# Performance work log

Measured on AMD Instinct MI355X. Metric: run time of the kernel, lower is better.

The kernel has to match this reference:

```python
import jax, jax.numpy as jnp
import numpy as np

B, S, D, H = 4, 2048, 1024, 16
HD = D // H

def setup_inputs() -> dict:
    key = jax.random.key(0)
    ks = jax.random.split(key, 10)
    s = 1.0 / np.sqrt(D)
    inp = {
        'x': jax.random.normal(ks[0], (B, S, D), dtype=jnp.float32),
        'attention_mask': jnp.ones((B, S), dtype=jnp.int32),
        'Wq': jax.random.uniform(ks[1], (D, D), jnp.float32, -s, s),
        'bq': jax.random.uniform(ks[2], (D,), jnp.float32, -s, s),
        'Wk': jax.random.uniform(ks[3], (D, D), jnp.float32, -s, s),
        'bk': jax.random.uniform(ks[4], (D,), jnp.float32, -s, s),
        'Wv': jax.random.uniform(ks[5], (D, D), jnp.float32, -s, s),
        'bv': jax.random.uniform(ks[6], (D,), jnp.float32, -s, s),
        'Wo': jax.random.uniform(ks[7], (D, D), jnp.float32, -s, s),
        'bo': jax.random.uniform(ks[8], (D,), jnp.float32, -s, s),
    }
    return inp

def reference(x, Wq, bq, Wk, bk, Wv, bv, Wo, bo, attention_mask):
    scale = HD ** -0.5
    # torch Linear: y = x @ W^T + b
    def proj(W, b):
        return (x @ W.T + b).reshape(B, S, H, HD).transpose(0, 2, 1, 3)  # [B,H,S,hd]
    q = proj(Wq, bq)
    k = proj(Wk, bk)
    v = proj(Wv, bv)
    scores = jnp.einsum('bhqd,bhkd->bhqk', q, k) * scale  # [B,H,S,S]
    causal = jnp.triu(jnp.ones((S, S), dtype=bool), k=1)
    scores = jnp.where(causal, -jnp.inf, scores)
    pad = (attention_mask == 0)[:, None, None, :]  # [B,1,1,S]
    scores = jnp.where(pad, jnp.float32(-1e9), scores)
    probs = jax.nn.softmax(scores, axis=-1)
    out = jnp.einsum('bhqk,bhkd->bhqd', probs, v)  # [B,H,S,hd]
    out = out.transpose(0, 2, 1, 3).reshape(B, S, D)
    return out @ Wo.T + bo
```

## Files before the change

kernel.cpp:

```cpp
#include <hip/hip_runtime.h>
#include <hip/hip_bf16.h>

typedef unsigned short u16;
typedef float f32x4 __attribute__((ext_vector_type(4)));
typedef __bf16 bf16x8 __attribute__((ext_vector_type(8)));

#define BB 4
#define SS 2048
#define DD 1024
#define HH 16
#define HDD 64
#define MM (BB*SS)

__device__ __forceinline__ u16 f2bf(float f){
    union { float f; unsigned int i; } v; v.f = f;
    unsigned int i = v.i;
    return (u16)((i + 0x7FFFu + ((i >> 16) & 1u)) >> 16);
}
__device__ __forceinline__ ushort2 pk2(float a, float b){
    union { __hip_bfloat162 h; ushort2 u; } v;
    float2 t; t.x = a; t.y = b;
    v.h = __float22bfloat162_rn(t);
    return v.u;
}
__device__ __forceinline__ ushort4 pk4(float a, float b, float c, float d){
    ushort2 lo = pk2(a, b), hi = pk2(c, d);
    ushort4 r; r.x = lo.x; r.y = lo.y; r.z = hi.x; r.w = hi.y;
    return r;
}
__device__ __forceinline__ void gl2lds16(const void* g, void* l){
    __builtin_amdgcn_global_load_lds(
        (const __attribute__((address_space(1))) void*)g,
        (__attribute__((address_space(3))) void*)l, 16, 0, 0);
}

__device__ __forceinline__ void cvt8(const float* __restrict__ src,
                                     u16* __restrict__ dst, size_t i)
{
    const float4 a = *(const float4*)&src[i];
    const float4 b = *(const float4*)&src[i + 4];
    ushort4 lo = pk4(a.x, a.y, a.z, a.w);
    ushort4 hi = pk4(b.x, b.y, b.z, b.w);
    uint4 o;
    o.x = (unsigned)lo.x | ((unsigned)lo.y << 16);
    o.y = (unsigned)lo.z | ((unsigned)lo.w << 16);
    o.z = (unsigned)hi.x | ((unsigned)hi.y << 16);
    o.w = (unsigned)hi.z | ((unsigned)hi.w << 16);
    *(uint4*)&dst[i] = o;
}

__global__ __launch_bounds__(256) void cvt_k(const float* __restrict__ src,
                                             u16* __restrict__ dst)
{
    const size_t i = ((size_t)blockIdx.x * 256 + threadIdx.x) * 8;
    cvt8(src, dst, i);
}

__global__ __launch_bounds__(256) void cvtw3_k(
    const float* __restrict__ W0, const float* __restrict__ W1,
    const float* __restrict__ W2, u16* __restrict__ dst)
{
    const float* src = blockIdx.y == 0 ? W0 : (blockIdx.y == 1 ? W1 : W2);
    u16* d = dst + (size_t)blockIdx.y * (size_t)DD * DD;
    const size_t i = ((size_t)blockIdx.x * 256 + threadIdx.x) * 8;
    cvt8(src, d, i);
}

__global__ __launch_bounds__(256) void cvtw1_k(const float* __restrict__ W,
                                               u16* __restrict__ dst)
{
    const size_t i = ((size_t)blockIdx.x * 256 + threadIdx.x) * 8;
    cvt8(W, dst, i);
}

__device__ __forceinline__ void gemm_core(const u16* __restrict__ Wb,
                                          const u16* __restrict__ Act,
                                          f32x4 (&acc)[4][4],
                                          u16 (&At)[2][256 * 32],
                                          u16 (&Bt)[2][128 * 32],
                                          int n0, int m0, int tid)
{
    const int lane = tid & 63, w = tid >> 6;
    const int quad = lane >> 4, l15 = lane & 15;
    const int wn2 = w & 3, wm2 = w >> 2;
    const int arow = lane >> 2;
    const int acol = (lane & 3) * 8;

    auto STG = [&](int bi, int kt) {
        const int kk = kt * 32;
        #pragma unroll
        for (int c0 = 0; c0 < 3; ++c0) {
            const int c = w * 3 + c0;
            if (c < 16) {
                gl2lds16(&Wb[(size_t)(n0 + c * 16 + arow) * DD + kk + acol],
                         &At[bi][c * 512]);
            } else {
                const int cb = c - 16;
                gl2lds16(&Act[(size_t)(m0 + cb * 16 + arow) * DD + kk + acol],
                         &Bt[bi][cb * 512]);
            }
        }
    };
    auto CMP = [&](int bi) {
        bf16x8 af[4], bfr[4];
        #pragma unroll
        for (int i = 0; i < 4; ++i)
            af[i] = *(const bf16x8*)&At[bi][(wn2 * 64 + i * 16 + l15) * 32 + quad * 8];
        #pragma unroll
        for (int j = 0; j < 4; ++j)
            bfr[j] = *(const bf16x8*)&Bt[bi][(wm2 * 64 + j * 16 + l15) * 32 + quad * 8];
        #pragma unroll
        for (int i = 0; i < 4; ++i)
            #pragma unroll
            for (int j = 0; j < 4; ++j)
                acc[i][j] = __builtin_amdgcn_mfma_f32_16x16x32_bf16(af[i], bfr[j], acc[i][j], 0, 0, 0);
    };

    STG(0, 0);
    __syncthreads();
    #pragma unroll 1
    for (int i = 0; i < 15; ++i) {
        STG(1, 2 * i + 1);
        CMP(0);
        __syncthreads();
        STG(0, 2 * i + 2);
        CMP(1);
        __syncthreads();
    }
    STG(1, 31);
    CMP(0);
    __syncthreads();
    CMP(1);
}

__global__ __launch_bounds__(512, 2) void gemm_qkv_k(
    const u16* __restrict__ x,
    const float* __restrict__ bq, const float* __restrict__ bk,
    const float* __restrict__ bv,
    const u16* __restrict__ Wqb, const u16* __restrict__ Wkb,
    const u16* __restrict__ Wvb,
    u16* __restrict__ Q, u16* __restrict__ K, u16* __restrict__ V)
{
    __shared__ alignas(16) u16 At[2][256 * 32];
    __shared__ alignas(16) u16 Bt[2][128 * 32];
    const int tid = threadIdx.x, lane = tid & 63, w = tid >> 6;
    const int quad = lane >> 4, l15 = lane & 15;
    const int wn2 = w & 3, wm2 = w >> 2;
    const int z = blockIdx.z;
    const u16* Wmb = z == 0 ? Wqb : (z == 1 ? Wkb : Wvb);
    const float* bias = z == 0 ? bq : (z == 1 ? bk : bv);
    u16* Out = z == 0 ? Q : (z == 1 ? K : V);
    const int m0 = blockIdx.x * 128, n0 = blockIdx.y * 256;

    f32x4 acc[4][4];
    #pragma unroll
    for (int i = 0; i < 4; ++i)
        #pragma unroll
        for (int j = 0; j < 4; ++j) acc[i][j] = (f32x4)(0.0f);

    gemm_core(Wmb, x, acc, At, Bt, n0, m0, tid);

    f32x4 bsv[4];
    #pragma unroll
    for (int i = 0; i < 4; ++i)
        bsv[i] = *(const f32x4*)&bias[n0 + wn2 * 64 + i * 16 + quad * 4];

    const int b = m0 / SS;
    const int h = (n0 + wn2 * 64) / HDD;
    const size_t base = ((size_t)(b * HH + h)) * SS * HDD;
    if (z == 2) {
        #pragma unroll
        for (int i = 0; i < 4; ++i) {
            #pragma unroll
            for (int r = 0; r < 4; ++r) {
                const int hd = i * 16 + quad * 4 + r;
                const float bb = bsv[i][r];
                #pragma unroll
                for (int j = 0; j < 4; ++j) {
                    const int s = (m0 % SS) + wm2 * 64 + j * 16 + l15;
                    Out[base + (size_t)hd * SS + s] = f2bf(acc[i][j][r] + bb);
                }
            }
        }
    } else {
        #pragma unroll
        for (int j = 0; j < 4; ++j) {
            const int s = (m0 % SS) + wm2 * 64 + j * 16 + l15;
            #pragma unroll
            for (int i = 0; i < 4; ++i) {
                *(ushort4*)&Out[base + (size_t)s * HDD + i * 16 + quad * 4] =
                    pk4(acc[i][j][0] + bsv[i][0], acc[i][j][1] + bsv[i][1],
                        acc[i][j][2] + bsv[i][2], acc[i][j][3] + bsv[i][3]);
            }
        }
    }
}

__global__ __launch_bounds__(512, 2) void gemm_out_k(
    const u16* __restrict__ A, const float* __restrict__ bo,
    const u16* __restrict__ Wob, float* __restrict__ Out)
{
    __shared__ alignas(16) u16 At[2][256 * 32];
    __shared__ alignas(16) u16 Bt[2][128 * 32];
    const int tid = threadIdx.x, lane = tid & 63, w = tid >> 6;
    const int quad = lane >> 4, l15 = lane & 15;
    const int wn2 = w & 3, wm2 = w >> 2;
    const int m0 = blockIdx.x * 128, n0 = blockIdx.y * 256;

    f32x4 acc[4][4];
    #pragma unroll
    for (int i = 0; i < 4; ++i)
        #pragma unroll
        for (int j = 0; j < 4; ++j) acc[i][j] = (f32x4)(0.0f);

    gemm_core(Wob, A, acc, At, Bt, n0, m0, tid);

    f32x4 bsv[4];
    #pragma unroll
    for (int i = 0; i < 4; ++i)
        bsv[i] = *(const f32x4*)&bo[n0 + wn2 * 64 + i * 16 + quad * 4];

    #pragma unroll
    for (int j = 0; j < 4; ++j) {
        const int m = m0 + wm2 * 64 + j * 16 + l15;
        #pragma unroll
        for (int i = 0; i < 4; ++i) {
            float4 f;
            f.x = acc[i][j][0] + bsv[i][0];
            f.y = acc[i][j][1] + bsv[i][1];
            f.z = acc[i][j][2] + bsv[i][2];
            f.w = acc[i][j][3] + bsv[i][3];
            *(float4*)&Out[(size_t)m * DD + n0 + wn2 * 64 + i * 16 + quad * 4] = f;
        }
    }
}

#define QT 128
#define KT 64

#define LOG2E 1.4426950408889634f

__device__ __forceinline__ int swz128(int row, int bcol){
    return row * 128 + (bcol ^ ((row & 7) << 4));
}

__global__ __launch_bounds__(256, 2) void attn_k(
    const u16* __restrict__ Q, const u16* __restrict__ K,
    const u16* __restrict__ V, const int* __restrict__ mask,
    u16* __restrict__ AO)
{
    __shared__ alignas(16) u16 QPs[QT * 64];
    __shared__ alignas(16) u16 Ks[KT * 64];
    __shared__ alignas(16) u16 Vs[KT * 64];
    __shared__ float padf[KT];

    const int tid = threadIdx.x, lane = tid & 63, w = tid >> 6;
    const int quad = lane >> 4, l15 = lane & 15;
    const int bh = blockIdx.x;
    const int y = blockIdx.y;
    const int qt = (y < 8) ? (15 - y) : (y - 8);
    const int b = bh >> 4, h = bh & 15;
    const int q0 = qt * QT;
    const size_t hoff = (size_t)bh * SS * HDD;
    const u16* Qh = Q + hoff;
    const u16* Kh = K + hoff;
    const u16* Vt = V + hoff;
    const int nkt = (q0 + QT) / KT;
    const float scale2 = 0.125f * LOG2E;
    const int wrow_end = q0 + w * 32 + 32;

    const int vrow = lane >> 3;
    const int dbcol = (((lane & 7) ^ vrow) << 4);

    for (int c = tid; c < QT * 8; c += 256) {
        const int row = c >> 3, cc = c & 7;
        *(uint4*)((char*)QPs + swz128(row, cc * 16)) =
            *(const uint4*)&Qh[(size_t)(q0 + row) * HDD + cc * 8];
    }
    __syncthreads();

    bf16x8 bQ[2][2];
    #pragma unroll
    for (int j = 0; j < 2; ++j)
        #pragma unroll
        for (int ks = 0; ks < 2; ++ks)
            bQ[j][ks] = *(const bf16x8*)((const char*)QPs +
                swz128(w * 32 + j * 16 + l15, ks * 64 + quad * 16));

    float m_run[2] = { -1e30f, -1e30f };
    float l_run[2] = { 0.f, 0.f };
    f32x4 o[4][2];
    #pragma unroll
    for (int i = 0; i < 4; ++i)
        #pragma unroll
        for (int j = 0; j < 2; ++j) o[i][j] = (f32x4)(0.0f);

    int pm = 1;
    if (tid < KT) pm = mask[b * SS + tid];

    for (int kt = 0; kt < nkt; ++kt) {
        const int kt0 = kt * KT;
        __syncthreads();

        #pragma unroll
        for (int c0 = 0; c0 < 2; ++c0) {
            const int c = w * 2 + c0;
            gl2lds16((const char*)Kh + (size_t)(kt0 + c * 8 + vrow) * 128 + dbcol,
                     (char*)Ks + c * 1024);
            gl2lds16((const char*)Vt + ((size_t)(c * 8 + vrow) * SS + kt0) * 2 + dbcol,
                     (char*)Vs + c * 1024);
        }
        if (tid < KT) padf[tid] = (pm == 0) ? -1e9f : 0.0f;
        __syncthreads();

        if (tid < KT && kt + 1 < nkt) pm = mask[b * SS + kt0 + KT + tid];

        if (kt0 < wrow_end) {
        f32x4 sc[4][2];
        #pragma unroll
        for (int i = 0; i < 4; ++i)
            #pragma unroll
            for (int j = 0; j < 2; ++j) sc[i][j] = (f32x4)(0.0f);
        __builtin_amdgcn_s_setprio(1);
        #pragma unroll
        for (int ks = 0; ks < 2; ++ks) {
            bf16x8 aK[4];
            #pragma unroll
            for (int i = 0; i < 4; ++i)
                aK[i] = *(const bf16x8*)((const char*)Ks +
                    swz128(i * 16 + l15, ks * 64 + quad * 16));
            #pragma unroll
            for (int i = 0; i < 4; ++i)
                #pragma unroll
                for (int j = 0; j < 2; ++j)
                    sc[i][j] = __builtin_amdgcn_mfma_f32_16x16x32_bf16(aK[i], bQ[j][ks], sc[i][j], 0, 0, 0);
        }
        __builtin_amdgcn_s_setprio(0);

        f32x4 pb[4];
        #pragma unroll
        for (int i = 0; i < 4; ++i)
            pb[i] = *(const f32x4*)&padf[i * 16 + quad * 4];

        #pragma unroll
        for (int j = 0; j < 2; ++j) {
            const int qrow = q0 + w * 32 + j * 16 + l15;
            const bool needC = (kt0 + KT - 1) > (q0 + w * 32 + j * 16);
            float mx = -1e9f;
            if (needC) {
                #pragma unroll
                for (int i = 0; i < 4; ++i)
                    #pragma unroll
                    for (int r = 0; r < 4; ++r) {
                        const int kpg = kt0 + i * 16 + quad * 4 + r;
                        float s = fmaf(sc[i][j][r], scale2, pb[i][r]);
                        s = (kpg > qrow) ? -1e9f : s;
                        sc[i][j][r] = s; mx = fmaxf(mx, s);
                    }
            } else {
                #pragma unroll
                for (int i = 0; i < 4; ++i)
                    #pragma unroll
                    for (int r = 0; r < 4; ++r) {
                        float s = fmaf(sc[i][j][r], scale2, pb[i][r]);
                        sc[i][j][r] = s; mx = fmaxf(mx, s);
                    }
            }
            mx = fmaxf(mx, __shfl_xor(mx, 16, 64));
            mx = fmaxf(mx, __shfl_xor(mx, 32, 64));
            float nm = m_run[j];
            if (!__all(mx <= nm + 8.f)) {
                nm = fmaxf(nm, mx);
                const float alpha = __builtin_exp2f(m_run[j] - nm);
                m_run[j] = nm;
                l_run[j] *= alpha;
                #pragma unroll
                for (int i = 0; i < 4; ++i)
                    #pragma unroll
                    for (int r = 0; r < 4; ++r) o[i][j][r] *= alpha;
            }
            float rs = 0.f;
            #pragma unroll
            for (int i = 0; i < 4; ++i) {
                float p0 = __builtin_exp2f(sc[i][j][0] - nm);
                float p1 = __builtin_exp2f(sc[i][j][1] - nm);
                float p2 = __builtin_exp2f(sc[i][j][2] - nm);
                float p3 = __builtin_exp2f(sc[i][j][3] - nm);
                rs += (p0 + p1) + (p2 + p3);
                *(ushort4*)((char*)QPs + swz128(w * 32 + j * 16 + l15, i * 32 + quad * 8)) =
                    pk4(p0, p1, p2, p3);
            }
            l_run[j] += rs;
        }
        asm volatile("s_waitcnt lgkmcnt(0)" ::: "memory");

        __builtin_amdgcn_s_setprio(1);
        #pragma unroll
        for (int ks = 0; ks < 2; ++ks) {
            bf16x8 aV[4], bP[2];
            #pragma unroll
            for (int i = 0; i < 4; ++i)
                aV[i] = *(const bf16x8*)((const char*)Vs +
                    swz128(i * 16 + l15, ks * 64 + quad * 16));
            #pragma unroll
            for (int j = 0; j < 2; ++j)
                bP[j] = *(const bf16x8*)((const char*)QPs +
                    swz128(w * 32 + j * 16 + l15, ks * 64 + quad * 16));
            #pragma unroll
            for (int i = 0; i < 4; ++i)
                #pragma unroll
                for (int j = 0; j < 2; ++j)
                    o[i][j] = __builtin_amdgcn_mfma_f32_16x16x32_bf16(aV[i], bP[j], o[i][j], 0, 0, 0);
        }
        __builtin_amdgcn_s_setprio(0);
        }
    }

    #pragma unroll
    for (int j = 0; j < 2; ++j) {
        float l = l_run[j];
        l += __shfl_xor(l, 16, 64);
        l += __shfl_xor(l, 32, 64);
        const float inv = (l > 0.f) ? (1.f / l) : 0.f;
        const int s = q0 + w * 32 + j * 16 + l15;
        const size_t rb = ((size_t)(b * SS + s)) * DD + h * HDD;
        #pragma unroll
        for (int i = 0; i < 4; ++i)
            *(ushort4*)&AO[rb + i * 16 + quad * 4] =
                pk4(o[i][j][0] * inv, o[i][j][1] * inv, o[i][j][2] * inv, o[i][j][3] * inv);
    }
}

extern "C" void kernel_launch(void* const* d_in, const int* in_sizes, int n_in,
                              void* d_out, int out_size, void* d_ws, size_t ws_size,
                              hipStream_t stream)
{
    const float* x  = (const float*)d_in[0];
    const int* mask = (const int*)d_in[1];
    const float* Wq = (const float*)d_in[2];
    const float* bq = (const float*)d_in[3];
    const float* Wk = (const float*)d_in[4];
    const float* bk = (const float*)d_in[5];
    const float* Wv = (const float*)d_in[6];
    const float* bv = (const float*)d_in[7];
    const float* Wo = (const float*)d_in[8];
    const float* bo = (const float*)d_in[9];
    float* out = (float*)d_out;

    u16* ws = (u16*)d_ws;
    const size_t NE = (size_t)MM * DD;
    const size_t WE = (size_t)DD * DD;
    if (ws_size < 4 * NE * sizeof(u16)) return;

    u16* Qb = ws;
    u16* Kb = ws + NE;
    u16* Vb = ws + 2 * NE;
    u16* Ab = ws + 3 * NE;

    u16* Wscr = (u16*)d_out;

    dim3 blk(256);
    cvt_k<<<dim3(NE / 2048), blk, 0, stream>>>(x, Ab);
    cvtw3_k<<<dim3(WE / 2048, 3), blk, 0, stream>>>(Wq, Wk, Wv, Wscr);
    gemm_qkv_k<<<dim3(MM / 128, DD / 256, 3), dim3(512), 0, stream>>>(
        Ab, bq, bk, bv, Wscr, Wscr + WE, Wscr + 2 * WE, Qb, Kb, Vb);
    attn_k<<<dim3(BB * HH, SS / QT), dim3(256), 0, stream>>>(Qb, Kb, Vb, mask, Ab);
    cvtw1_k<<<dim3(WE / 2048), blk, 0, stream>>>(Wo, Qb);
    gemm_out_k<<<dim3(MM / 128, DD / 256), dim3(512), 0, stream>>>(Ab, bo, Qb, out);
}
```

Measured before the change: 297.6 us.

## Fuse fp32-to-bf16 conversion into GEMM tile staging, drop separate convert kernels

Removes the three standalone conversion kernels for x, the QKV weights and Wo. The GEMMs now load fp32 tiles directly and convert them to bf16 in registers before writing to LDS. This saves launches and the bf16 round trip through global memory. In exchange, staging now moves twice the bytes per tile, uses synchronous register loads instead of async global-to-LDS copies, and repeats the conversion for every block that reads the same tile.

```diff
diff --git a/kernel.cpp b/kernel.cpp
--- a/kernel.cpp
+++ b/kernel.cpp
@@ -33,12 +33,9 @@
         (const __attribute__((address_space(1))) void*)g,
         (__attribute__((address_space(3))) void*)l, 16, 0, 0);
 }
-
-__device__ __forceinline__ void cvt8(const float* __restrict__ src,
-                                     u16* __restrict__ dst, size_t i)
-{
-    const float4 a = *(const float4*)&src[i];
-    const float4 b = *(const float4*)&src[i + 4];
+__device__ __forceinline__ uint4 cvt8pack(const float* __restrict__ src){
+    const float4 a = *(const float4*)src;
+    const float4 b = *(const float4*)(src + 4);
     ushort4 lo = pk4(a.x, a.y, a.z, a.w);
     ushort4 hi = pk4(b.x, b.y, b.z, b.w);
     uint4 o;
@@ -46,35 +43,13 @@
     o.y = (unsigned)lo.z | ((unsigned)lo.w << 16);
     o.z = (unsigned)hi.x | ((unsigned)hi.y << 16);
     o.w = (unsigned)hi.z | ((unsigned)hi.w << 16);
-    *(uint4*)&dst[i] = o;
-}
-
-__global__ __launch_bounds__(256) void cvt_k(const float* __restrict__ src,
-                                             u16* __restrict__ dst)
-{
-    const size_t i = ((size_t)blockIdx.x * 256 + threadIdx.x) * 8;
-    cvt8(src, dst, i);
-}
-
-__global__ __launch_bounds__(256) void cvtw3_k(
-    const float* __restrict__ W0, const float* __restrict__ W1,
-    const float* __restrict__ W2, u16* __restrict__ dst)
-{
-    const float* src = blockIdx.y == 0 ? W0 : (blockIdx.y == 1 ? W1 : W2);
-    u16* d = dst + (size_t)blockIdx.y * (size_t)DD * DD;
-    const size_t i = ((size_t)blockIdx.x * 256 + threadIdx.x) * 8;
-    cvt8(src, d, i);
-}
-
-__global__ __launch_bounds__(256) void cvtw1_k(const float* __restrict__ W,
-                                               u16* __restrict__ dst)
-{
-    const size_t i = ((size_t)blockIdx.x * 256 + threadIdx.x) * 8;
-    cvt8(W, dst, i);
-}
-
-__device__ __forceinline__ void gemm_core(const u16* __restrict__ Wb,
-                                          const u16* __restrict__ Act,
+    return o;
+}
+
+template<bool ACTBF>
+__device__ __forceinline__ void gemm_core(const float* __restrict__ Wf,
+                                          const float* __restrict__ ActF,
+                                          const u16*  __restrict__ ActB,
                                           f32x4 (&acc)[4][4],
                                           u16 (&At)[2][256 * 32],
                                           u16 (&Bt)[2][128 * 32],
@@ -89,16 +64,19 @@
     auto STG = [&](int bi, int kt) {
         const int kk = kt * 32;
         #pragma unroll
-        for (int c0 = 0; c0 < 3; ++c0) {
-            const int c = w * 3 + c0;
-            if (c < 16) {
-                gl2lds16(&Wb[(size_t)(n0 + c * 16 + arow) * DD + kk + acol],
-                         &At[bi][c * 512]);
-            } else {
-                const int cb = c - 16;
-                gl2lds16(&Act[(size_t)(m0 + cb * 16 + arow) * DD + kk + acol],
-                         &Bt[bi][cb * 512]);
-            }
+        for (int it = 0; it < 2; ++it) {
+            const int u = tid + it * 512;
+            const int row = u >> 2, g = u & 3;
+            *(uint4*)&At[bi][row * 32 + g * 8] =
+                cvt8pack(&Wf[(size_t)(n0 + row) * DD + kk + g * 8]);
+        }
+        if (ACTBF) {
+            gl2lds16(&ActB[(size_t)(m0 + w * 16 + arow) * DD + kk + acol],
+                     &Bt[bi][w * 512]);
+        } else {
+            const int row = tid >> 2, g = tid & 3;
+            *(uint4*)&Bt[bi][row * 32 + g * 8] =
+                cvt8pack(&ActF[(size_t)(m0 + row) * DD + kk + g * 8]);
         }
     };
     auto CMP = [&](int bi) {
@@ -134,11 +112,11 @@
 }
 
 __global__ __launch_bounds__(512, 2) void gemm_qkv_k(
-    const u16* __restrict__ x,
+    const float* __restrict__ x,
     const float* __restrict__ bq, const float* __restrict__ bk,
     const float* __restrict__ bv,
-    const u16* __restrict__ Wqb, const u16* __restrict__ Wkb,
-    const u16* __restrict__ Wvb,
+    const float* __restrict__ Wq, const float* __restrict__ Wk,
+    const float* __restrict__ Wv,
     u16* __restrict__ Q, u16* __restrict__ K, u16* __restrict__ V)
 {
     __shared__ alignas(16) u16 At[2][256 * 32];
@@ -147,7 +125,7 @@
     const int quad = lane >> 4, l15 = lane & 15;
     const int wn2 = w & 3, wm2 = w >> 2;
     const int z = blockIdx.z;
-    const u16* Wmb = z == 0 ? Wqb : (z == 1 ? Wkb : Wvb);
+    const float* Wm = z == 0 ? Wq : (z == 1 ? Wk : Wv);
     const float* bias = z == 0 ? bq : (z == 1 ? bk : bv);
     u16* Out = z == 0 ? Q : (z == 1 ? K : V);
     const int m0 = blockIdx.x * 128, n0 = blockIdx.y * 256;
@@ -158,7 +136,7 @@
         #pragma unroll
         for (int j = 0; j < 4; ++j) acc[i][j] = (f32x4)(0.0f);
 
-    gemm_core(Wmb, x, acc, At, Bt, n0, m0, tid);
+    gemm_core<false>(Wm, x, nullptr, acc, At, Bt, n0, m0, tid);
 
     f32x4 bsv[4];
     #pragma unroll
@@ -198,7 +176,7 @@
 
 __global__ __launch_bounds__(512, 2) void gemm_out_k(
     const u16* __restrict__ A, const float* __restrict__ bo,
-    const u16* __restrict__ Wob, float* __restrict__ Out)
+    const float* __restrict__ Wo, float* __restrict__ Out)
 {
     __shared__ alignas(16) u16 At[2][256 * 32];
     __shared__ alignas(16) u16 Bt[2][128 * 32];
@@ -213,7 +191,7 @@
         #pragma unroll
         for (int j = 0; j < 4; ++j) acc[i][j] = (f32x4)(0.0f);
 
-    gemm_core(Wob, A, acc, At, Bt, n0, m0, tid);
+    gemm_core<true>(Wo, nullptr, A, acc, At, Bt, n0, m0, tid);
 
     f32x4 bsv[4];
     #pragma unroll
@@ -449,7 +427,6 @@
 
     u16* ws = (u16*)d_ws;
     const size_t NE = (size_t)MM * DD;
-    const size_t WE = (size_t)DD * DD;
     if (ws_size < 4 * NE * sizeof(u16)) return;
 
     u16* Qb = ws;
@@ -457,14 +434,8 @@
     u16* Vb = ws + 2 * NE;
     u16* Ab = ws + 3 * NE;
 
-    u16* Wscr = (u16*)d_out;
-
-    dim3 blk(256);
-    cvt_k<<<dim3(NE / 2048), blk, 0, stream>>>(x, Ab);
-    cvtw3_k<<<dim3(WE / 2048, 3), blk, 0, stream>>>(Wq, Wk, Wv, Wscr);
     gemm_qkv_k<<<dim3(MM / 128, DD / 256, 3), dim3(512), 0, stream>>>(
-        Ab, bq, bk, bv, Wscr, Wscr + WE, Wscr + 2 * WE, Qb, Kb, Vb);
+        x, bq, bk, bv, Wq, Wk, Wv, Qb, Kb, Vb);
     attn_k<<<dim3(BB * HH, SS / QT), dim3(256), 0, stream>>>(Qb, Kb, Vb, mask, Ab);
-    cvtw1_k<<<dim3(WE / 2048), blk, 0, stream>>>(Wo, Qb);
-    gemm_out_k<<<dim3(MM / 128, DD / 256), dim3(512), 0, stream>>>(Ab, bo, Qb, out);
-}
+    gemm_out_k<<<dim3(MM / 128, DD / 256), dim3(512), 0, stream>>>(Ab, bo, Wo, out);
+}
```

Result: slower. 377.0 us (+26.7%).
